# Kernel tuning notes

Hardware: AMD Instinct MI355X
Metric: run time of the kernel (lower is better)

Reference implementation:

```python
import jax, jax.numpy as jnp
import numpy as np

N = 200000
X_SIZE = 256
H_SIZE = 256


def setup_inputs() -> dict:
    key = jax.random.key(0)
    k1, k2, k3, k4, k5 = jax.random.split(key, 5)
    x = jax.random.normal(k1, (N, X_SIZE), dtype=jnp.float32)
    Uh_sum = jax.random.normal(k2, (N, 3 * H_SIZE), dtype=jnp.float32)
    fc_sum = jax.random.normal(k3, (N, H_SIZE), dtype=jnp.float32)
    W_iou = jax.random.normal(k4, (3 * H_SIZE, X_SIZE), dtype=jnp.float32) * (X_SIZE ** -0.5)
    b_iou = jnp.zeros((1, 3 * H_SIZE), dtype=jnp.float32)
    W_f = jax.random.normal(k5, (H_SIZE, X_SIZE), dtype=jnp.float32) * (X_SIZE ** -0.5)
    b_f = jnp.zeros((1, H_SIZE), dtype=jnp.float32)
    return {"x": x, "Uh_sum": Uh_sum, "fc_sum": fc_sum,
            "W_iou": W_iou, "b_iou": b_iou, "W_f": W_f, "b_f": b_f}


def reference(x, Uh_sum, fc_sum, W_iou, b_iou, W_f, b_f):
    # init_matrices: per-node input projections
    x_iou = jnp.einsum('nd,kd->nk', x, W_iou) + b_iou   # [N, 3H]
    x_f = jnp.einsum('nd,kd->nk', x, W_f) + b_f         # [N, H]
    # apply_node_func: fused gate update with aggregated child messages
    iou = x_iou + Uh_sum
    i, o, u = jnp.split(iou, 3, axis=1)
    c = jax.nn.sigmoid(i) * jnp.tanh(u) + fc_sum
    h = jax.nn.sigmoid(o) * jnp.tanh(c)
    return h, c, x_f
```

## Files before the change

kernel.cpp:

```cpp
#include <hip/hip_runtime.h>
#include <hip/hip_bf16.h>
#include <stdint.h>


typedef __attribute__((ext_vector_type(8))) short bf16x8;
typedef __attribute__((ext_vector_type(4))) float f4v;

#define N_ROWS 200000
#define TILES 12500
#define XSTR 258

__device__ __forceinline__ bf16x8 pack8(f4v a, f4v b) {
    union { __hip_bfloat162 h2[4]; bf16x8 v; } u;
    u.h2[0] = __float22bfloat162_rn(make_float2(a.x, a.y));
    u.h2[1] = __float22bfloat162_rn(make_float2(a.z, a.w));
    u.h2[2] = __float22bfloat162_rn(make_float2(b.x, b.y));
    u.h2[3] = __float22bfloat162_rn(make_float2(b.z, b.w));
    return u.v;
}
__device__ __forceinline__ float fsig(float x) { return 1.0f / (1.0f + __expf(-x)); }
__device__ __forceinline__ float ftanh(float x) {
    float e = __expf(2.0f * x);
    return 1.0f - 2.0f / (e + 1.0f);
}

__global__ __launch_bounds__(512)
__attribute__((amdgpu_waves_per_eu(2, 2)))
void treelstm_main(const float* __restrict__ x,
                   const float* __restrict__ Uh,
                   const float* __restrict__ fc,
                   const float* __restrict__ W_iou,
                   const float* __restrict__ b_iou,
                   const float* __restrict__ W_f,
                   const float* __restrict__ b_f,
                   float* __restrict__ out) {
    __shared__ float xlds[2][16 * XSTR];

    const int tid   = threadIdx.x;
    const int lane  = tid & 63;
    const int w     = tid >> 6;
    const int q     = lane >> 4;
    const int bcol  = lane & 15;
    const int half  = blockIdx.x >> 7;
    const int phase = blockIdx.x & 127;
    const int sl    = half * 8 + w;
    const int kb    = sl * 16 + q * 4;
    const int C     = sl * 16 + bcol;

    const f4v bi  = *(const f4v*)&b_iou[kb];
    const f4v bo  = *(const f4v*)&b_iou[256 + kb];
    const f4v bu  = *(const f4v*)&b_iou[512 + kb];
    const f4v bf4 = *(const f4v*)&b_f[kb];

    bf16x8 wreg[32];
#pragma unroll
    for (int g = 0; g < 4; ++g) {
        const float* wr = (g < 3) ? (W_iou + (size_t)(g * 256 + C) * 256)
                                  : (W_f + (size_t)C * 256);
#pragma unroll
        for (int ks = 0; ks < 8; ++ks) {
            const f4v p0 = *(const f4v*)(wr + ks * 32 + q * 8);
            const f4v p1 = *(const f4v*)(wr + ks * 32 + q * 8 + 4);
            wreg[g * 8 + ks] = pack8(p0, p1);
        }
    }

    float* out_h = out;
    float* out_c = out + (size_t)N_ROWS * 256;
    float* out_f = out + 2 * (size_t)N_ROWS * 256;

    auto STAGE = [&](int t, int buf) {
#pragma unroll
        for (int rr = 0; rr < 2; ++rr) {
            const int r = 2 * w + rr;
            const float* src = x + (size_t)(t * 16 + r) * 256 + lane * 4;
            __builtin_amdgcn_global_load_lds(
                (const __attribute__((address_space(1))) uint32_t*)src,
                (__attribute__((address_space(3))) uint32_t*)&xlds[buf][r * XSTR],
                16, 0, 0);
        }
        __builtin_amdgcn_sched_barrier(0);
    };

    f4v uhi, uho, uhu, fcv;
    auto LOADUH = [&](int tt) {
        const float* uh = Uh + (size_t)(tt * 16 + bcol) * 768 + kb;
        uhi = __builtin_nontemporal_load((const f4v*)uh);
        uho = __builtin_nontemporal_load((const f4v*)(uh + 256));
        uhu = __builtin_nontemporal_load((const f4v*)(uh + 512));
        fcv = __builtin_nontemporal_load((const f4v*)(fc + (size_t)(tt * 16 + bcol) * 256 + kb));
    };

    int t = phase, buf = 0;
    STAGE(t, 0);
    LOADUH(t);
    asm volatile("s_waitcnt vmcnt(4)" ::: "memory");
    __builtin_amdgcn_s_barrier();
    __builtin_amdgcn_sched_barrier(0);

    while (true) {
        const int tn = t + 128;
        const bool more = (tn < TILES);
        if (more) STAGE(tn, buf ^ 1);

        f4v acc0 = bi, acc1 = bo, acc2 = bu, acc3 = bf4;
#pragma unroll
        for (int ks = 0; ks < 8; ++ks) {
            const f4v p0 = *(const f4v*)&xlds[buf][bcol * XSTR + ks * 32 + q * 8];
            const f4v p1 = *(const f4v*)&xlds[buf][bcol * XSTR + ks * 32 + q * 8 + 4];
            const bf16x8 xf = pack8(p0, p1);
            acc0 = __builtin_amdgcn_mfma_f32_16x16x32_bf16(wreg[0 * 8 + ks], xf, acc0, 0, 0, 0);
            acc1 = __builtin_amdgcn_mfma_f32_16x16x32_bf16(wreg[1 * 8 + ks], xf, acc1, 0, 0, 0);
            acc2 = __builtin_amdgcn_mfma_f32_16x16x32_bf16(wreg[2 * 8 + ks], xf, acc2, 0, 0, 0);
            acc3 = __builtin_amdgcn_mfma_f32_16x16x32_bf16(wreg[3 * 8 + ks], xf, acc3, 0, 0, 0);
        }

        const int n = t * 16 + bcol;
        f4v cc, hh, ff;
        cc.x = fsig(acc0.x + uhi.x) * ftanh(acc2.x + uhu.x) + fcv.x;
        cc.y = fsig(acc0.y + uhi.y) * ftanh(acc2.y + uhu.y) + fcv.y;
        cc.z = fsig(acc0.z + uhi.z) * ftanh(acc2.z + uhu.z) + fcv.z;
        cc.w = fsig(acc0.w + uhi.w) * ftanh(acc2.w + uhu.w) + fcv.w;
        hh.x = fsig(acc1.x + uho.x) * ftanh(cc.x);
        hh.y = fsig(acc1.y + uho.y) * ftanh(cc.y);
        hh.z = fsig(acc1.z + uho.z) * ftanh(cc.z);
        hh.w = fsig(acc1.w + uho.w) * ftanh(cc.w);
        ff.x = acc3.x; ff.y = acc3.y; ff.z = acc3.z; ff.w = acc3.w;
        const size_t oidx = (size_t)n * 256 + kb;
        __builtin_nontemporal_store(hh, (f4v*)(out_h + oidx));
        __builtin_nontemporal_store(cc, (f4v*)(out_c + oidx));
        __builtin_nontemporal_store(ff, (f4v*)(out_f + oidx));

        if (!more) break;

        LOADUH(tn);
        asm volatile("s_waitcnt vmcnt(7)" ::: "memory");
        __builtin_amdgcn_s_barrier();
        __builtin_amdgcn_sched_barrier(0);
        t = tn; buf ^= 1;
    }
}

extern "C" void kernel_launch(void* const* d_in, const int* in_sizes, int n_in,
                              void* d_out, int out_size, void* d_ws, size_t ws_size,
                              hipStream_t stream) {
    const float* x     = (const float*)d_in[0];
    const float* Uh    = (const float*)d_in[1];
    const float* fc    = (const float*)d_in[2];
    const float* W_iou = (const float*)d_in[3];
    const float* b_iou = (const float*)d_in[4];
    const float* W_f   = (const float*)d_in[5];
    const float* b_f   = (const float*)d_in[6];
    float* out = (float*)d_out;

    treelstm_main<<<256, 512, 0, stream>>>(x, Uh, fc, W_iou, b_iou, W_f, b_f, out);
}
```

Before: 418.7 us.

## Deepen pipeline to two tiles in flight with four LDS buffers

```diff
diff --git a/kernel.cpp b/kernel.cpp
--- a/kernel.cpp
+++ b/kernel.cpp
@@ -9,6 +9,8 @@
 #define N_ROWS 200000
 #define TILES 12500
 #define XSTR 258
+#define VMW(N) asm volatile("s_waitcnt vmcnt(" #N ")" ::: "memory")
+#define SBR() __builtin_amdgcn_sched_barrier(0)
 
 __device__ __forceinline__ bf16x8 pack8(f4v a, f4v b) {
     union { __hip_bfloat162 h2[4]; bf16x8 v; } u;
@@ -34,7 +36,7 @@
                    const float* __restrict__ W_f,
                    const float* __restrict__ b_f,
                    float* __restrict__ out) {
-    __shared__ float xlds[2][16 * XSTR];
+    __shared__ float xlds[4][16 * XSTR];
 
     const int tid   = threadIdx.x;
     const int lane  = tid & 63;
@@ -47,10 +49,10 @@
     const int kb    = sl * 16 + q * 4;
     const int C     = sl * 16 + bcol;
 
-    const f4v bi  = *(const f4v*)&b_iou[kb];
-    const f4v bo  = *(const f4v*)&b_iou[256 + kb];
-    const f4v bu  = *(const f4v*)&b_iou[512 + kb];
-    const f4v bf4 = *(const f4v*)&b_f[kb];
+    const f4v bI = *(const f4v*)&b_iou[kb];
+    const f4v bO = *(const f4v*)&b_iou[256 + kb];
+    const f4v bU = *(const f4v*)&b_iou[512 + kb];
+    const f4v bF = *(const f4v*)&b_f[kb];
 
     bf16x8 wreg[32];
 #pragma unroll
@@ -64,80 +66,100 @@
             wreg[g * 8 + ks] = pack8(p0, p1);
         }
     }
+    VMW(0); SBR();
 
     float* out_h = out;
     float* out_c = out + (size_t)N_ROWS * 256;
     float* out_f = out + 2 * (size_t)N_ROWS * 256;
 
-    auto STAGE = [&](int t, int buf) {
+    const int cnt   = (TILES - phase + 127) >> 7;
+    const int pairs = cnt >> 1;
+    const int tail  = cnt & 1;
+
+    auto TN = [&](int j) { const int jj = (j < cnt) ? j : (cnt - 1);
+                           return phase + (jj << 7); };
+
+    auto STAGE = [&](int t, int rb) {
 #pragma unroll
         for (int rr = 0; rr < 2; ++rr) {
             const int r = 2 * w + rr;
             const float* src = x + (size_t)(t * 16 + r) * 256 + lane * 4;
             __builtin_amdgcn_global_load_lds(
                 (const __attribute__((address_space(1))) uint32_t*)src,
-                (__attribute__((address_space(3))) uint32_t*)&xlds[buf][r * XSTR],
+                (__attribute__((address_space(3))) uint32_t*)&xlds[rb][r * XSTR],
                 16, 0, 0);
         }
-        __builtin_amdgcn_sched_barrier(0);
+        SBR();
     };
 
-    f4v uhi, uho, uhu, fcv;
-    auto LOADUH = [&](int tt) {
-        const float* uh = Uh + (size_t)(tt * 16 + bcol) * 768 + kb;
-        uhi = __builtin_nontemporal_load((const f4v*)uh);
-        uho = __builtin_nontemporal_load((const f4v*)(uh + 256));
-        uhu = __builtin_nontemporal_load((const f4v*)(uh + 512));
-        fcv = __builtin_nontemporal_load((const f4v*)(fc + (size_t)(tt * 16 + bcol) * 256 + kb));
+    auto LOADUH = [&](int t, f4v& ui, f4v& uo, f4v& uu, f4v& fv) {
+        const float* uh = Uh + (size_t)(t * 16 + bcol) * 768 + kb;
+        ui = __builtin_nontemporal_load((const f4v*)uh);
+        uo = __builtin_nontemporal_load((const f4v*)(uh + 256));
+        uu = __builtin_nontemporal_load((const f4v*)(uh + 512));
+        fv = __builtin_nontemporal_load((const f4v*)(fc + (size_t)(t * 16 + bcol) * 256 + kb));
     };
 
-    int t = phase, buf = 0;
-    STAGE(t, 0);
-    LOADUH(t);
-    asm volatile("s_waitcnt vmcnt(4)" ::: "memory");
-    __builtin_amdgcn_s_barrier();
-    __builtin_amdgcn_sched_barrier(0);
-
-    while (true) {
-        const int tn = t + 128;
-        const bool more = (tn < TILES);
-        if (more) STAGE(tn, buf ^ 1);
-
-        f4v acc0 = bi, acc1 = bo, acc2 = bu, acc3 = bf4;
+    auto WORK = [&](int rb, int t, const f4v& ui, const f4v& uo,
+                    const f4v& uu, const f4v& fv) {
+        f4v a0 = bI, a1 = bO, a2 = bU, a3 = bF;
 #pragma unroll
         for (int ks = 0; ks < 8; ++ks) {
-            const f4v p0 = *(const f4v*)&xlds[buf][bcol * XSTR + ks * 32 + q * 8];
-            const f4v p1 = *(const f4v*)&xlds[buf][bcol * XSTR + ks * 32 + q * 8 + 4];
+            const f4v p0 = *(const f4v*)&xlds[rb][bcol * XSTR + ks * 32 + q * 8];
+            const f4v p1 = *(const f4v*)&xlds[rb][bcol * XSTR + ks * 32 + q * 8 + 4];
             const bf16x8 xf = pack8(p0, p1);
-            acc0 = __builtin_amdgcn_mfma_f32_16x16x32_bf16(wreg[0 * 8 + ks], xf, acc0, 0, 0, 0);
-            acc1 = __builtin_amdgcn_mfma_f32_16x16x32_bf16(wreg[1 * 8 + ks], xf, acc1, 0, 0, 0);
-            acc2 = __builtin_amdgcn_mfma_f32_16x16x32_bf16(wreg[2 * 8 + ks], xf, acc2, 0, 0, 0);
-            acc3 = __builtin_amdgcn_mfma_f32_16x16x32_bf16(wreg[3 * 8 + ks], xf, acc3, 0, 0, 0);
+            a0 = __builtin_amdgcn_mfma_f32_16x16x32_bf16(wreg[0 * 8 + ks], xf, a0, 0, 0, 0);
+            a1 = __builtin_amdgcn_mfma_f32_16x16x32_bf16(wreg[1 * 8 + ks], xf, a1, 0, 0, 0);
+            a2 = __builtin_amdgcn_mfma_f32_16x16x32_bf16(wreg[2 * 8 + ks], xf, a2, 0, 0, 0);
+            a3 = __builtin_amdgcn_mfma_f32_16x16x32_bf16(wreg[3 * 8 + ks], xf, a3, 0, 0, 0);
         }
-
         const int n = t * 16 + bcol;
         f4v cc, hh, ff;
-        cc.x = fsig(acc0.x + uhi.x) * ftanh(acc2.x + uhu.x) + fcv.x;
-        cc.y = fsig(acc0.y + uhi.y) * ftanh(acc2.y + uhu.y) + fcv.y;
-        cc.z = fsig(acc0.z + uhi.z) * ftanh(acc2.z + uhu.z) + fcv.z;
-        cc.w = fsig(acc0.w + uhi.w) * ftanh(acc2.w + uhu.w) + fcv.w;
-        hh.x = fsig(acc1.x + uho.x) * ftanh(cc.x);
-        hh.y = fsig(acc1.y + uho.y) * ftanh(cc.y);
-        hh.z = fsig(acc1.z + uho.z) * ftanh(cc.z);
-        hh.w = fsig(acc1.w + uho.w) * ftanh(cc.w);
-        ff.x = acc3.x; ff.y = acc3.y; ff.z = acc3.z; ff.w = acc3.w;
+        cc.x = fsig(a0.x + ui.x) * ftanh(a2.x + uu.x) + fv.x;
+        cc.y = fsig(a0.y + ui.y) * ftanh(a2.y + uu.y) + fv.y;
+        cc.z = fsig(a0.z + ui.z) * ftanh(a2.z + uu.z) + fv.z;
+        cc.w = fsig(a0.w + ui.w) * ftanh(a2.w + uu.w) + fv.w;
+        hh.x = fsig(a1.x + uo.x) * ftanh(cc.x);
+        hh.y = fsig(a1.y + uo.y) * ftanh(cc.y);
+        hh.z = fsig(a1.z + uo.z) * ftanh(cc.z);
+        hh.w = fsig(a1.w + uo.w) * ftanh(cc.w);
+        ff.x = a3.x; ff.y = a3.y; ff.z = a3.z; ff.w = a3.w;
         const size_t oidx = (size_t)n * 256 + kb;
-        __builtin_nontemporal_store(hh, (f4v*)(out_h + oidx));
-        __builtin_nontemporal_store(cc, (f4v*)(out_c + oidx));
-        __builtin_nontemporal_store(ff, (f4v*)(out_f + oidx));
+        *(f4v*)(out_h + oidx) = hh;
+        *(f4v*)(out_c + oidx) = cc;
+        *(f4v*)(out_f + oidx) = ff;
+    };
 
-        if (!more) break;
+    f4v uhiA, uhoA, uhuA, fcvA, uhiB, uhoB, uhuB, fcvB;
 
-        LOADUH(tn);
-        asm volatile("s_waitcnt vmcnt(7)" ::: "memory");
-        __builtin_amdgcn_s_barrier();
-        __builtin_amdgcn_sched_barrier(0);
-        t = tn; buf ^= 1;
+    STAGE(TN(0), 0); LOADUH(TN(0), uhiA, uhoA, uhuA, fcvA);
+    STAGE(TN(1), 1); LOADUH(TN(1), uhiB, uhoB, uhuB, fcvB);
+    VMW(10);
+    __builtin_amdgcn_s_barrier(); SBR();
+
+    for (int i = 0; i < pairs; ++i) {
+        const int j0 = 2 * i;
+        const int rA = (i & 1) ? 2 : 0;
+        const int rB = rA + 1;
+        const int sA = (i & 1) ? 0 : 2;
+        const int sB = sA + 1;
+
+        STAGE(TN(j0 + 2), sA);
+        WORK(rA, TN(j0), uhiA, uhoA, uhuA, fcvA);
+        LOADUH(TN(j0 + 2), uhiA, uhoA, uhuA, fcvA);
+        if (i == 0) { VMW(13); } else { VMW(16); }
+        __builtin_amdgcn_s_barrier(); SBR();
+
+        STAGE(TN(j0 + 3), sB);
+        WORK(rB, TN(j0 + 1), uhiB, uhoB, uhuB, fcvB);
+        LOADUH(TN(j0 + 3), uhiB, uhoB, uhuB, fcvB);
+        VMW(16);
+        __builtin_amdgcn_s_barrier(); SBR();
+    }
+
+    if (tail) {
+        const int rA = (pairs & 1) ? 2 : 0;
+        WORK(rA, TN(cnt - 1), uhiA, uhoA, uhuA, fcvA);
     }
 }
 
```

Result: faster. 362.8 us (-13.3%).
